# Kernel optimization log

Measured on AMD Instinct MI355X. Metric: run time of the kernel, lower is better.

## Reference

```python
import jax, jax.numpy as jnp
import numpy as np

K_NEIGHBORS = 3


def setup_inputs() -> dict:
    key = jax.random.key(0)
    ks = jax.random.split(key, 16)
    B, N = 8, 2048
    s = 0.05
    p = {
        "x": jax.random.normal(ks[0], (B, N, 4), dtype=jnp.float32),
        "W1": jax.random.normal(ks[1], (4, 64), dtype=jnp.float32) * s,
        "b1": jnp.zeros((64,), jnp.float32),
        "W2": jax.random.normal(ks[2], (64, 64), dtype=jnp.float32) * s,
        "b2": jnp.zeros((64,), jnp.float32),
        "Wm": jax.random.normal(ks[3], (64, 64), dtype=jnp.float32) * s,
        "bm": jnp.zeros((64,), jnp.float32),
        "Wu1": jax.random.normal(ks[4], (128, 128), dtype=jnp.float32) * s,
        "bu1": jnp.zeros((128,), jnp.float32),
        "Wu2": jax.random.normal(ks[5], (128, 128), dtype=jnp.float32) * s,
        "bu2": jnp.zeros((128,), jnp.float32),
        "Wmean": jax.random.normal(ks[6], (128, 2), dtype=jnp.float32) * s,
        "bmean": jnp.zeros((2,), jnp.float32),
        "Wv": jax.random.normal(ks[7], (128, 1), dtype=jnp.float32) * s,
        "bv": jnp.zeros((1,), jnp.float32),
        "log_std": jnp.zeros((2,), jnp.float32),
    }
    return p


def reference(x, W1, b1, W2, b2, Wm, bm, Wu1, bu1, Wu2, bu2, Wmean, bmean, Wv, bv, log_std):
    # node MLP: [B,N,4] -> [B,N,64]
    h = jax.nn.relu(x @ W1 + b1)
    h = jax.nn.relu(h @ W2 + b2)
    # pairwise squared distances without materializing [B,N,N,64] diff:
    # ||a-b||^2 = ||a||^2 + ||b||^2 - 2 a.b  (same math as diff.pow(2).sum(-1))
    sq = jnp.sum(h * h, axis=-1)  # [B,N]
    gram = jnp.einsum("bnd,bmd->bnm", h, h)  # [B,N,N]
    dist = sq[:, :, None] + sq[:, None, :] - 2.0 * gram  # [B,N,N]
    # k smallest (ascending) = top_k of negated dist; drop self (index 0)
    _, idx = jax.lax.top_k(-dist, K_NEIGHBORS + 1)  # [B,N,K+1]
    knn_idx = idx[:, :, 1:]  # [B,N,K]
    # gather neighbor features: [B,N,K,64]
    neigh = jax.vmap(lambda hb, ib: hb[ib])(h, knn_idx)
    # msg MLP + mean over neighbors
    msgs = jax.nn.relu(neigh @ Wm + bm).mean(axis=2)  # [B,N,64]
    hc = jnp.concatenate([h, msgs], axis=-1)  # [B,N,128]
    u = jax.nn.relu(hc @ Wu1 + bu1)
    u = jax.nn.relu(u @ Wu2 + bu2)
    return (u @ Wmean + bmean, jnp.exp(log_std), u @ Wv + bv)
```

## Files before the change

### kernel.cpp

```cpp
#include <hip/hip_runtime.h>
#include <math.h>

#define NB 8
#define NN 2048

typedef short bf16x8 __attribute__((ext_vector_type(8)));
typedef float f32x4  __attribute__((ext_vector_type(4)));

__device__ __forceinline__ f32x4 mfma16(uint4 a, uint4 b, f32x4 c) {
    return __builtin_amdgcn_mfma_f32_16x16x32_bf16(
        __builtin_bit_cast(bf16x8, a), __builtin_bit_cast(bf16x8, b), c, 0, 0, 0);
}

__device__ __forceinline__ float bf2f(unsigned short u) {
    unsigned int t = ((unsigned int)u) << 16;
    return __builtin_bit_cast(float, t);
}

__device__ __forceinline__ unsigned short f2bf_rne(float f) {
    unsigned int u = __builtin_bit_cast(unsigned int, f);
    return (unsigned short)((u + 0x7FFFu + ((u >> 16) & 1u)) >> 16);
}

__device__ __forceinline__ unsigned int rne_pair(unsigned int a, unsigned int b, unsigned int c) {
    float lo = bf2f((unsigned short)(a & 0xFFFF)) + bf2f((unsigned short)(b & 0xFFFF)) + bf2f((unsigned short)(c & 0xFFFF));
    float hi = bf2f((unsigned short)(a >> 16)) + bf2f((unsigned short)(b >> 16)) + bf2f((unsigned short)(c >> 16));
    return (unsigned int)f2bf_rne(lo) | ((unsigned int)f2bf_rne(hi) << 16);
}
__device__ __forceinline__ uint4 rne_merge(uint4 a, uint4 b, uint4 c) {
    return make_uint4(rne_pair(a.x, b.x, c.x), rne_pair(a.y, b.y, c.y),
                      rne_pair(a.z, b.z, c.z), rne_pair(a.w, b.w, c.w));
}

#define INS4(vv, ii, d, j) {                                      \
    bool c0 = (d < vv.x) || (d == vv.x && j < ii.x);              \
    bool c1 = (d < vv.y) || (d == vv.y && j < ii.y);              \
    bool c2 = (d < vv.z) || (d == vv.z && j < ii.z);              \
    bool c3 = (d < vv.w) || (d == vv.w && j < ii.w);              \
    vv.w = c3 ? (c2 ? vv.z : d) : vv.w; ii.w = c3 ? (c2 ? ii.z : j) : ii.w; \
    vv.z = c2 ? (c1 ? vv.y : d) : vv.z; ii.z = c2 ? (c1 ? ii.y : j) : ii.z; \
    vv.y = c1 ? (c0 ? vv.x : d) : vv.y; ii.y = c1 ? (c0 ? ii.x : j) : ii.y; \
    vv.x = c0 ? d : vv.x;               ii.x = c0 ? j : ii.x; }

#define INS4S(vv, ii, d, j) {                                     \
    bool c0 = (d < vv.x); bool c1 = (d < vv.y);                   \
    bool c2 = (d < vv.z); bool c3 = (d < vv.w);                   \
    vv.w = c3 ? (c2 ? vv.z : d) : vv.w; ii.w = c3 ? (c2 ? ii.z : j) : ii.w; \
    vv.z = c2 ? (c1 ? vv.y : d) : vv.z; ii.z = c2 ? (c1 ? ii.y : j) : ii.z; \
    vv.y = c1 ? (c0 ? vv.x : d) : vv.y; ii.y = c1 ? (c0 ? ii.x : j) : ii.y; \
    vv.x = c0 ? d : vv.x;               ii.x = c0 ? j : ii.x; }

__global__ __launch_bounds__(256) void k_embed(
    const float* __restrict__ x, const float* __restrict__ W1, const float* __restrict__ b1,
    const float* __restrict__ W2, const float* __restrict__ b2,
    uint4* __restrict__ HsF, float* __restrict__ sqv)
{
    __shared__ float w2s[4096];
    __shared__ float h1s[4][4][64];
    __shared__ unsigned short sh[3 * 16 * 72];
    int tid = threadIdx.x;
    for (int q = tid; q < 4096; q += 256) w2s[q] = W2[q];
    int wave = tid >> 6, lane = tid & 63;
    int nbase = blockIdx.x * 16 + wave * 4;
    float w10 = W1[lane], w11 = W1[64 + lane], w12 = W1[128 + lane], w13 = W1[192 + lane];
    float b1l = b1[lane];
    #pragma unroll
    for (int v = 0; v < 4; v++) {
        float4 xv = reinterpret_cast<const float4*>(x)[nbase + v];
        h1s[wave][v][lane] = fmaxf(b1l + xv.x * w10 + xv.y * w11 + xv.z * w12 + xv.w * w13, 0.f);
    }
    __syncthreads();
    float b2l = b2[lane];
    float a0 = b2l, a1 = b2l, a2 = b2l, a3 = b2l;
    for (int k = 0; k < 64; k++) {
        float w = w2s[k * 64 + lane];
        a0 += h1s[wave][0][k] * w; a1 += h1s[wave][1][k] * w;
        a2 += h1s[wave][2][k] * w; a3 += h1s[wave][3][k] * w;
    }
    float hvs[4] = {fmaxf(a0, 0.f), fmaxf(a1, 0.f), fmaxf(a2, 0.f), fmaxf(a3, 0.f)};
    #pragma unroll
    for (int v = 0; v < 4; v++) {
        float hval = hvs[v];
        long node = nbase + v;
        int row = wave * 4 + v;
        unsigned int u0 = __builtin_bit_cast(unsigned int, hval);
        unsigned short s0 = (unsigned short)(u0 >> 16);
        float f0 = __builtin_bit_cast(float, u0 & 0xFFFF0000u);
        float r1 = hval - f0;
        unsigned int u1 = __builtin_bit_cast(unsigned int, r1);
        unsigned short s1 = (unsigned short)(u1 >> 16);
        float f1 = __builtin_bit_cast(float, u1 & 0xFFFF0000u);
        float r2 = r1 - f1;
        unsigned short s2 = (unsigned short)(__builtin_bit_cast(unsigned int, r2) >> 16);
        sh[(0 * 16 + row) * 72 + lane] = s0;
        sh[(1 * 16 + row) * 72 + lane] = s1;
        sh[(2 * 16 + row) * 72 + lane] = s2;
        float s = hval * hval;
        #pragma unroll
        for (int m = 1; m < 64; m <<= 1) s += __shfl_xor(s, m, 64);
        if (lane == 0) sqv[node] = s;
    }
    __syncthreads();
    for (int q = tid; q < 384; q += 256) {
        int f = q >> 6, ln = q & 63;
        int s = f >> 1, hf = f & 1;
        int row = ln & 15, eb = hf * 32 + (ln >> 4) * 8;
        const unsigned short* sp = &sh[(s * 16 + row) * 72 + eb];
        unsigned int p0 = (unsigned int)sp[0] | ((unsigned int)sp[1] << 16);
        unsigned int p1 = (unsigned int)sp[2] | ((unsigned int)sp[3] << 16);
        unsigned int p2 = (unsigned int)sp[4] | ((unsigned int)sp[5] << 16);
        unsigned int p3 = (unsigned int)sp[6] | ((unsigned int)sp[7] << 16);
        HsF[((long)blockIdx.x * 6 + f) * 64 + ln] = make_uint4(p0, p1, p2, p3);
    }
}

__global__ __launch_bounds__(256, 3) void k_knn(
    const uint4* __restrict__ HsF, const float* __restrict__ sqv,
    float* __restrict__ pval, int* __restrict__ pidx)
{
    __shared__ float smv[4][1056];
    __shared__ int   smi[4][1056];

    int tid = threadIdx.x;
    int wave = tid >> 6, lane = tid & 63;
    int l15 = lane & 15, quad = lane >> 4;

    int bx = blockIdx.x;
    int js = bx & 3;
    int gquad = (bx >> 2) & 31;
    int b = bx >> 7;
    int gwb = gquad * 4 + wave;
    long g = (long)b * 128 + gwb;
    const float* sqb = sqv + ((long)b << 11);

    uint4 A[6];
    #pragma unroll
    for (int f = 0; f < 6; f++)
        A[f] = HsF[(g * 6 + f) * 64 + lane];

    float4 val[4]; int4 idx[4];
    #pragma unroll
    for (int r = 0; r < 4; r++) {
        val[r] = make_float4(3.4e38f, 3.4e38f, 3.4e38f, 3.4e38f);
        idx[r] = make_int4(0x7fffffff, 0x7fffffff, 0x7fffffff, 0x7fffffff);
    }

#define LOADB(B, SJ, G) {                                                     \
    long fb = ((long)b * 128 + (G)) * 6;                                      \
    _Pragma("unroll")                                                         \
    for (int f = 0; f < 6; f++)                                               \
        B[f] = HsF[(fb + f) * 64 + lane];                                     \
    SJ = sqb[(G) * 16 + l15]; }

#define COMPUTE(B, SJ, G) {                                                   \
    int j = (G) * 16 + l15;                                                   \
    f32x4 acc = {0.f, 0.f, 0.f, 0.f};                                         \
    _Pragma("unroll")                                                         \
    for (int hf = 0; hf < 2; hf++) {                                          \
        acc = mfma16(A[hf],     B[hf],     acc);                              \
        acc = mfma16(A[hf],     B[2 + hf], acc);                              \
        acc = mfma16(A[2 + hf], B[hf],     acc);                              \
        acc = mfma16(A[2 + hf], B[2 + hf], acc);                              \
        acc = mfma16(A[hf],     B[4 + hf], acc);                              \
        acc = mfma16(A[4 + hf], B[hf],     acc);                              \
    }                                                                         \
    _Pragma("unroll")                                                         \
    for (int r = 0; r < 4; r++) {                                             \
        float d = fmaf(-2.f, acc[r], SJ);                                     \
        INS4S(val[r], idx[r], d, j);                                          \
    } }

    int jg0 = js * 32;
    uint4 B0[6], B1[6];
    float sj0, sj1;
    LOADB(B0, sj0, jg0);
    #pragma unroll 1
    for (int t = 0; t < 16; t++) {
        int ga = jg0 + t * 2;
        int gbn = ga + 1;
        int gc = jg0 + ((t * 2 + 2) & 31);
        LOADB(B1, sj1, gbn);
        COMPUTE(B0, sj0, ga);
        LOADB(B0, sj0, gc);
        COMPUTE(B1, sj1, gbn);
    }

    float* mv = smv[wave]; int* mi = smi[wave];
    #pragma unroll
    for (int r = 0; r < 4; r++) {
        int base = (quad * 4 + r) * 65 + l15 * 4;
        mv[base + 0] = val[r].x; mv[base + 1] = val[r].y;
        mv[base + 2] = val[r].z; mv[base + 3] = val[r].w;
        mi[base + 0] = idx[r].x; mi[base + 1] = idx[r].y;
        mi[base + 2] = idx[r].z; mi[base + 3] = idx[r].w;
    }
    __syncthreads();
    float4 fv = make_float4(3.4e38f, 3.4e38f, 3.4e38f, 3.4e38f);
    int4   fi = make_int4(0x7fffffff, 0x7fffffff, 0x7fffffff, 0x7fffffff);
    #pragma unroll
    for (int tt = 0; tt < 4; tt++) {
        int base = l15 * 65 + (quad * 4 + tt) * 4;
        #pragma unroll
        for (int k = 0; k < 4; k++) {
            float d = mv[base + k];
            int j = mi[base + k];
            INS4(fv, fi, d, j);
        }
    }
    #pragma unroll
    for (int m = 16; m <= 32; m <<= 1) {
        float ov0 = __shfl_xor(fv.x, m, 64), ov1 = __shfl_xor(fv.y, m, 64);
        float ov2 = __shfl_xor(fv.z, m, 64), ov3 = __shfl_xor(fv.w, m, 64);
        int   oi0 = __shfl_xor(fi.x, m, 64), oi1 = __shfl_xor(fi.y, m, 64);
        int   oi2 = __shfl_xor(fi.z, m, 64), oi3 = __shfl_xor(fi.w, m, 64);
        INS4(fv, fi, ov0, oi0); INS4(fv, fi, ov1, oi1);
        INS4(fv, fi, ov2, oi2); INS4(fv, fi, ov3, oi3);
    }
    if (quad == 0) {
        long gi = ((long)b << 11) + gwb * 16 + l15;
        pval[gi * 16 + js * 4 + 0] = fv.x; pidx[gi * 16 + js * 4 + 0] = fi.x;
        pval[gi * 16 + js * 4 + 1] = fv.y; pidx[gi * 16 + js * 4 + 1] = fi.y;
        pval[gi * 16 + js * 4 + 2] = fv.z; pidx[gi * 16 + js * 4 + 2] = fi.z;
        pval[gi * 16 + js * 4 + 3] = fv.w; pidx[gi * 16 + js * 4 + 3] = fi.w;
    }
}

__global__ __launch_bounds__(256) void k_knn_merge(
    const float* __restrict__ pval, const int* __restrict__ pidx, int* __restrict__ knn)
{
    int gi = blockIdx.x * 256 + threadIdx.x;
    float4 fv = make_float4(3.4e38f, 3.4e38f, 3.4e38f, 3.4e38f);
    int4   fi = make_int4(0x7fffffff, 0x7fffffff, 0x7fffffff, 0x7fffffff);
    #pragma unroll
    for (int t = 0; t < 16; t++) {
        float d = pval[(long)gi * 16 + t];
        int j = pidx[(long)gi * 16 + t];
        INS4(fv, fi, d, j);
    }
    int* o = knn + (long)gi * 3;
    o[0] = fi.y; o[1] = fi.z; o[2] = fi.w;
}

__global__ __launch_bounds__(256) void k_head(
    const uint4* __restrict__ HsF, const int* __restrict__ knn,
    const float* __restrict__ Wm, const float* __restrict__ bm,
    const float* __restrict__ Wu1, const float* __restrict__ bu1,
    const float* __restrict__ Wu2, const float* __restrict__ bu2,
    const float* __restrict__ Wmean, const float* __restrict__ bmean,
    const float* __restrict__ Wv, const float* __restrict__ bv,
    const float* __restrict__ log_std,
    float* __restrict__ out_mean, float* __restrict__ out_std, float* __restrict__ out_val)
{
    __shared__ __align__(16) uint4 wmf[8 * 64];
    __shared__ __align__(16) uint4 wuf[32 * 64];
    __shared__ __align__(16) unsigned short hcT[4][16 * 136];

    int tid = threadIdx.x;
    int wave = tid >> 6, lane = tid & 63;
    int l15 = lane & 15, quad = lane >> 4;
    long g = blockIdx.x * 4 + wave;
    int b = (int)(g >> 7);

    for (int q = tid; q < 512; q += 256) {
        int fi2 = q >> 6, ln = q & 63;
        int fg = fi2 >> 1, hf = fi2 & 1;
        int fr = ln & 15, qd = ln >> 4;
        unsigned int p[4];
        #pragma unroll
        for (int e2 = 0; e2 < 4; e2++) {
            unsigned int lo = f2bf_rne(Wm[(hf * 32 + qd * 8 + e2 * 2 + 0) * 64 + fg * 16 + fr]);
            unsigned int hi = f2bf_rne(Wm[(hf * 32 + qd * 8 + e2 * 2 + 1) * 64 + fg * 16 + fr]);
            p[e2] = lo | (hi << 16);
        }
        wmf[q] = make_uint4(p[0], p[1], p[2], p[3]);
    }
#define STAGE_WU(W) {                                                         \
    for (int q = tid; q < 2048; q += 256) {                                   \
        int fi2 = q >> 6, ln = q & 63;                                        \
        int fg = fi2 >> 2, kq = fi2 & 3;                                      \
        int fr = ln & 15, qd = ln >> 4;                                       \
        unsigned int p[4];                                                    \
        _Pragma("unroll")                                                     \
        for (int e2 = 0; e2 < 4; e2++) {                                      \
            unsigned int lo = f2bf_rne(W[(kq * 32 + qd * 8 + e2 * 2 + 0) * 128 + fg * 16 + fr]); \
            unsigned int hi = f2bf_rne(W[(kq * 32 + qd * 8 + e2 * 2 + 1) * 128 + fg * 16 + fr]); \
            p[e2] = lo | (hi << 16);                                          \
        }                                                                     \
        wuf[q] = make_uint4(p[0], p[1], p[2], p[3]);                          \
    } }
    STAGE_WU(Wu1)

    uint4 hA[2];
    #pragma unroll
    for (int hf = 0; hf < 2; hf++)
        hA[hf] = rne_merge(HsF[(g * 6 + hf) * 64 + lane],
                           HsF[(g * 6 + 2 + hf) * 64 + lane],
                           HsF[(g * 6 + 4 + hf) * 64 + lane]);
    uint4 nA[3][2];
    {
        int node0 = (int)g * 16 + l15;
        #pragma unroll
        for (int e = 0; e < 3; e++) {
            int jn = knn[node0 * 3 + e];
            long gj = (long)b * 128 + (jn >> 4);
            int ln2 = quad * 16 + (jn & 15);
            #pragma unroll
            for (int hf = 0; hf < 2; hf++)
                nA[e][hf] = rne_merge(HsF[(gj * 6 + hf) * 64 + ln2],
                                      HsF[(gj * 6 + 2 + hf) * 64 + ln2],
                                      HsF[(gj * 6 + 4 + hf) * 64 + ln2]);
        }
    }
    #pragma unroll
    for (int hf = 0; hf < 2; hf++)
        *reinterpret_cast<uint4*>(&hcT[wave][l15 * 136 + hf * 32 + quad * 8]) = hA[hf];
    __syncthreads();

    {
        uint4 wm_r[4][2];
        #pragma unroll
        for (int fg = 0; fg < 4; fg++)
            #pragma unroll
            for (int hf = 0; hf < 2; hf++)
                wm_r[fg][hf] = wmf[(fg * 2 + hf) * 64 + lane];
        float bmv[4];
        #pragma unroll
        for (int fg = 0; fg < 4; fg++) bmv[fg] = bm[fg * 16 + l15];
        f32x4 msum[4];
        #pragma unroll
        for (int fg = 0; fg < 4; fg++) msum[fg] = (f32x4){0.f, 0.f, 0.f, 0.f};
        #pragma unroll
        for (int e = 0; e < 3; e++)
            #pragma unroll
            for (int fg = 0; fg < 4; fg++) {
                f32x4 c = {0.f, 0.f, 0.f, 0.f};
                c = mfma16(nA[e][0], wm_r[fg][0], c);
                c = mfma16(nA[e][1], wm_r[fg][1], c);
                #pragma unroll
                for (int r = 0; r < 4; r++) msum[fg][r] += fmaxf(c[r] + bmv[fg], 0.f);
            }
        #pragma unroll
        for (int fg = 0; fg < 4; fg++)
            #pragma unroll
            for (int r = 0; r < 4; r++)
                hcT[wave][(quad * 4 + r) * 136 + 64 + fg * 16 + l15] = f2bf_rne(msum[fg][r] * (1.f / 3.f));
    }
    __syncthreads();

    unsigned short u1s[8][4];
    {
        uint4 a1[4];
        #pragma unroll
        for (int kq = 0; kq < 4; kq++)
            a1[kq] = *reinterpret_cast<const uint4*>(&hcT[wave][l15 * 136 + kq * 32 + quad * 8]);
        #pragma unroll
        for (int fg = 0; fg < 8; fg++) {
            float bv1 = bu1[fg * 16 + l15];
            f32x4 c = {0.f, 0.f, 0.f, 0.f};
            #pragma unroll
            for (int kq = 0; kq < 4; kq++)
                c = mfma16(a1[kq], wuf[(fg * 4 + kq) * 64 + lane], c);
            #pragma unroll
            for (int r = 0; r < 4; r++) u1s[fg][r] = f2bf_rne(fmaxf(c[r] + bv1, 0.f));
        }
        #pragma unroll
        for (int fg = 0; fg < 8; fg++)
            #pragma unroll
            for (int r = 0; r < 4; r++)
                hcT[wave][(quad * 4 + r) * 136 + fg * 16 + l15] = u1s[fg][r];
    }
    __syncthreads();
    STAGE_WU(Wu2)
    __syncthreads();

    float u2v[8][4];
    {
        uint4 a2[4];
        #pragma unroll
        for (int kq = 0; kq < 4; kq++)
            a2[kq] = *reinterpret_cast<const uint4*>(&hcT[wave][l15 * 136 + kq * 32 + quad * 8]);
        #pragma unroll
        for (int fg = 0; fg < 8; fg++) {
            float bv2 = bu2[fg * 16 + l15];
            f32x4 c = {0.f, 0.f, 0.f, 0.f};
            #pragma unroll
            for (int kq = 0; kq < 4; kq++)
                c = mfma16(a2[kq], wuf[(fg * 4 + kq) * 64 + lane], c);
            #pragma unroll
            for (int r = 0; r < 4; r++) u2v[fg][r] = fmaxf(c[r] + bv2, 0.f);
        }
    }

    {
        float wm0[8], wm1[8], wvv[8];
        #pragma unroll
        for (int fg = 0; fg < 8; fg++) {
            int f = fg * 16 + l15;
            wm0[fg] = Wmean[f * 2 + 0];
            wm1[fg] = Wmean[f * 2 + 1];
            wvv[fg] = Wv[f];
        }
        float bm0 = bmean[0], bm1 = bmean[1], bv0 = bv[0];
        #pragma unroll
        for (int r = 0; r < 4; r++) {
            float p0 = 0.f, p1 = 0.f, p2 = 0.f;
            #pragma unroll
            for (int fg = 0; fg < 8; fg++) {
                p0 = fmaf(u2v[fg][r], wm0[fg], p0);
                p1 = fmaf(u2v[fg][r], wm1[fg], p1);
                p2 = fmaf(u2v[fg][r], wvv[fg], p2);
            }
            #pragma unroll
            for (int m = 1; m < 16; m <<= 1) {
                p0 += __shfl_xor(p0, m, 64);
                p1 += __shfl_xor(p1, m, 64);
                p2 += __shfl_xor(p2, m, 64);
            }
            if (l15 == 0) {
                int node = (int)g * 16 + quad * 4 + r;
                out_mean[node * 2 + 0] = p0 + bm0;
                out_mean[node * 2 + 1] = p1 + bm1;
                out_val[node] = p2 + bv0;
            }
        }
    }
    if (blockIdx.x == 0 && tid < 2) out_std[tid] = expf(log_std[tid]);
}

extern "C" void kernel_launch(void* const* d_in, const int* in_sizes, int n_in,
                              void* d_out, int out_size, void* d_ws, size_t ws_size,
                              hipStream_t stream) {
    const float* x     = (const float*)d_in[0];
    const float* W1    = (const float*)d_in[1];
    const float* b1    = (const float*)d_in[2];
    const float* W2    = (const float*)d_in[3];
    const float* b2    = (const float*)d_in[4];
    const float* Wm    = (const float*)d_in[5];
    const float* bm    = (const float*)d_in[6];
    const float* Wu1   = (const float*)d_in[7];
    const float* bu1   = (const float*)d_in[8];
    const float* Wu2   = (const float*)d_in[9];
    const float* bu2   = (const float*)d_in[10];
    const float* Wmean = (const float*)d_in[11];
    const float* bmean = (const float*)d_in[12];
    const float* Wv    = (const float*)d_in[13];
    const float* bv    = (const float*)d_in[14];
    const float* lstd  = (const float*)d_in[15];

    float* out = (float*)d_out;
    float* out_mean = out;
    float* out_std  = out + 32768;
    float* out_val  = out + 32770;

    uint4* HsF  = (uint4*)d_ws;
    float* sqv  = (float*)(HsF + (long)1024 * 6 * 64);
    int*   knn  = (int*)(sqv + 16384);
    float* pval = (float*)(knn + 16384 * 3);
    int*   pidx = (int*)(pval + (long)16384 * 16);

    k_embed<<<1024, 256, 0, stream>>>(x, W1, b1, W2, b2, HsF, sqv);
    k_knn<<<1024, 256, 0, stream>>>(HsF, sqv, pval, pidx);
    k_knn_merge<<<64, 256, 0, stream>>>(pval, pidx, knn);
    k_head<<<256, 256, 0, stream>>>(HsF, knn, Wm, bm, Wu1, bu1, Wu2, bu2,
                                    Wmean, bmean, Wv, bv, lstd,
                                    out_mean, out_std, out_val);
}
```

Baseline: 203.5 us.

## Fold kNN merge into head, pre-convert weights once, use shuffle-based top-4 reduction

Removes the separate k_knn_merge kernel. The kNN kernel now reduces its per-lane top-4 lists with xor shuffles instead of a shared-memory transpose and writes packed 64-bit (distance key, index) pairs. k_head merges the four partial lists with u64 comparisons and shuffles. Weight bf16 fragment conversion moves from every head block into a small prep kernel, and k_head reads the fragments from global memory instead of LDS. The kNN inner loop is now fully unrolled with no explicit double-buffering, which raises register pressure. The packed sort key keeps the tie-break by index.

```diff
diff --git a/kernel.cpp b/kernel.cpp
--- a/kernel.cpp
+++ b/kernel.cpp
@@ -6,6 +6,7 @@
 
 typedef short bf16x8 __attribute__((ext_vector_type(8)));
 typedef float f32x4  __attribute__((ext_vector_type(4)));
+typedef unsigned long long u64;
 
 __device__ __forceinline__ f32x4 mfma16(uint4 a, uint4 b, f32x4 c) {
     return __builtin_amdgcn_mfma_f32_16x16x32_bf16(
@@ -30,6 +31,12 @@
 __device__ __forceinline__ uint4 rne_merge(uint4 a, uint4 b, uint4 c) {
     return make_uint4(rne_pair(a.x, b.x, c.x), rne_pair(a.y, b.y, c.y),
                       rne_pair(a.z, b.z, c.z), rne_pair(a.w, b.w, c.w));
+}
+
+__device__ __forceinline__ u64 packdj(float d, int j) {
+    unsigned int u = __builtin_bit_cast(unsigned int, d);
+    unsigned int key = u ^ ((unsigned int)(((int)u) >> 31) | 0x80000000u);
+    return ((u64)key << 32) | (unsigned int)j;
 }
 
 #define INS4(vv, ii, d, j) {                                      \
@@ -49,6 +56,47 @@
     vv.z = c2 ? (c1 ? vv.y : d) : vv.z; ii.z = c2 ? (c1 ? ii.y : j) : ii.z; \
     vv.y = c1 ? (c0 ? vv.x : d) : vv.y; ii.y = c1 ? (c0 ? ii.x : j) : ii.y; \
     vv.x = c0 ? d : vv.x;               ii.x = c0 ? j : ii.x; }
+
+#define INSQ(a0, a1, a2, a3, p) {                                 \
+    bool c0 = (p) < a0; bool c1 = (p) < a1;                       \
+    bool c2 = (p) < a2; bool c3 = (p) < a3;                       \
+    a3 = c3 ? (c2 ? a2 : (p)) : a3;                               \
+    a2 = c2 ? (c1 ? a1 : (p)) : a2;                               \
+    a1 = c1 ? (c0 ? a0 : (p)) : a1;                               \
+    a0 = c0 ? (p) : a0; }
+
+__global__ __launch_bounds__(256) void k_wprep(
+    const float* __restrict__ Wm, const float* __restrict__ Wu1, const float* __restrict__ Wu2,
+    uint4* __restrict__ wfrag)
+{
+    int q = blockIdx.x * 256 + threadIdx.x;
+    int ln = q & 63;
+    int fr = ln & 15, qd = ln >> 4;
+    unsigned int p[4];
+    if (q < 512) {
+        int fi2 = q >> 6;
+        int fg = fi2 >> 1, hf = fi2 & 1;
+        #pragma unroll
+        for (int e2 = 0; e2 < 4; e2++) {
+            unsigned int lo = f2bf_rne(Wm[(hf * 32 + qd * 8 + e2 * 2 + 0) * 64 + fg * 16 + fr]);
+            unsigned int hi = f2bf_rne(Wm[(hf * 32 + qd * 8 + e2 * 2 + 1) * 64 + fg * 16 + fr]);
+            p[e2] = lo | (hi << 16);
+        }
+    } else {
+        int qq = q - 512;
+        const float* W = (qq < 2048) ? Wu1 : Wu2;
+        int q2 = qq & 2047;
+        int fi2 = q2 >> 6;
+        int fg = fi2 >> 2, kq = fi2 & 3;
+        #pragma unroll
+        for (int e2 = 0; e2 < 4; e2++) {
+            unsigned int lo = f2bf_rne(W[(kq * 32 + qd * 8 + e2 * 2 + 0) * 128 + fg * 16 + fr]);
+            unsigned int hi = f2bf_rne(W[(kq * 32 + qd * 8 + e2 * 2 + 1) * 128 + fg * 16 + fr]);
+            p[e2] = lo | (hi << 16);
+        }
+    }
+    wfrag[q] = make_uint4(p[0], p[1], p[2], p[3]);
+}
 
 __global__ __launch_bounds__(256) void k_embed(
     const float* __restrict__ x, const float* __restrict__ W1, const float* __restrict__ b1,
@@ -116,11 +164,8 @@
 
 __global__ __launch_bounds__(256, 3) void k_knn(
     const uint4* __restrict__ HsF, const float* __restrict__ sqv,
-    float* __restrict__ pval, int* __restrict__ pidx)
+    u64* __restrict__ pk)
 {
-    __shared__ float smv[4][1056];
-    __shared__ int   smi[4][1056];
-
     int tid = threadIdx.x;
     int wave = tid >> 6, lane = tid & 63;
     int l15 = lane & 15, quad = lane >> 4;
@@ -145,114 +190,68 @@
         idx[r] = make_int4(0x7fffffff, 0x7fffffff, 0x7fffffff, 0x7fffffff);
     }
 
-#define LOADB(B, SJ, G) {                                                     \
-    long fb = ((long)b * 128 + (G)) * 6;                                      \
-    _Pragma("unroll")                                                         \
-    for (int f = 0; f < 6; f++)                                               \
-        B[f] = HsF[(fb + f) * 64 + lane];                                     \
-    SJ = sqb[(G) * 16 + l15]; }
-
-#define COMPUTE(B, SJ, G) {                                                   \
-    int j = (G) * 16 + l15;                                                   \
-    f32x4 acc = {0.f, 0.f, 0.f, 0.f};                                         \
-    _Pragma("unroll")                                                         \
-    for (int hf = 0; hf < 2; hf++) {                                          \
-        acc = mfma16(A[hf],     B[hf],     acc);                              \
-        acc = mfma16(A[hf],     B[2 + hf], acc);                              \
-        acc = mfma16(A[2 + hf], B[hf],     acc);                              \
-        acc = mfma16(A[2 + hf], B[2 + hf], acc);                              \
-        acc = mfma16(A[hf],     B[4 + hf], acc);                              \
-        acc = mfma16(A[4 + hf], B[hf],     acc);                              \
-    }                                                                         \
-    _Pragma("unroll")                                                         \
-    for (int r = 0; r < 4; r++) {                                             \
-        float d = fmaf(-2.f, acc[r], SJ);                                     \
-        INS4S(val[r], idx[r], d, j);                                          \
-    } }
-
     int jg0 = js * 32;
-    uint4 B0[6], B1[6];
-    float sj0, sj1;
-    LOADB(B0, sj0, jg0);
-    #pragma unroll 1
-    for (int t = 0; t < 16; t++) {
-        int ga = jg0 + t * 2;
-        int gbn = ga + 1;
-        int gc = jg0 + ((t * 2 + 2) & 31);
-        LOADB(B1, sj1, gbn);
-        COMPUTE(B0, sj0, ga);
-        LOADB(B0, sj0, gc);
-        COMPUTE(B1, sj1, gbn);
-    }
-
-    float* mv = smv[wave]; int* mi = smi[wave];
-    #pragma unroll
-    for (int r = 0; r < 4; r++) {
-        int base = (quad * 4 + r) * 65 + l15 * 4;
-        mv[base + 0] = val[r].x; mv[base + 1] = val[r].y;
-        mv[base + 2] = val[r].z; mv[base + 3] = val[r].w;
-        mi[base + 0] = idx[r].x; mi[base + 1] = idx[r].y;
-        mi[base + 2] = idx[r].z; mi[base + 3] = idx[r].w;
-    }
-    __syncthreads();
-    float4 fv = make_float4(3.4e38f, 3.4e38f, 3.4e38f, 3.4e38f);
-    int4   fi = make_int4(0x7fffffff, 0x7fffffff, 0x7fffffff, 0x7fffffff);
-    #pragma unroll
-    for (int tt = 0; tt < 4; tt++) {
-        int base = l15 * 65 + (quad * 4 + tt) * 4;
-        #pragma unroll
-        for (int k = 0; k < 4; k++) {
-            float d = mv[base + k];
-            int j = mi[base + k];
-            INS4(fv, fi, d, j);
-        }
-    }
-    #pragma unroll
-    for (int m = 16; m <= 32; m <<= 1) {
-        float ov0 = __shfl_xor(fv.x, m, 64), ov1 = __shfl_xor(fv.y, m, 64);
-        float ov2 = __shfl_xor(fv.z, m, 64), ov3 = __shfl_xor(fv.w, m, 64);
-        int   oi0 = __shfl_xor(fi.x, m, 64), oi1 = __shfl_xor(fi.y, m, 64);
-        int   oi2 = __shfl_xor(fi.z, m, 64), oi3 = __shfl_xor(fi.w, m, 64);
-        INS4(fv, fi, ov0, oi0); INS4(fv, fi, ov1, oi1);
-        INS4(fv, fi, ov2, oi2); INS4(fv, fi, ov3, oi3);
-    }
-    if (quad == 0) {
-        long gi = ((long)b << 11) + gwb * 16 + l15;
-        pval[gi * 16 + js * 4 + 0] = fv.x; pidx[gi * 16 + js * 4 + 0] = fi.x;
-        pval[gi * 16 + js * 4 + 1] = fv.y; pidx[gi * 16 + js * 4 + 1] = fi.y;
-        pval[gi * 16 + js * 4 + 2] = fv.z; pidx[gi * 16 + js * 4 + 2] = fi.z;
-        pval[gi * 16 + js * 4 + 3] = fv.w; pidx[gi * 16 + js * 4 + 3] = fi.w;
-    }
-}
-
-__global__ __launch_bounds__(256) void k_knn_merge(
-    const float* __restrict__ pval, const int* __restrict__ pidx, int* __restrict__ knn)
-{
-    int gi = blockIdx.x * 256 + threadIdx.x;
-    float4 fv = make_float4(3.4e38f, 3.4e38f, 3.4e38f, 3.4e38f);
-    int4   fi = make_int4(0x7fffffff, 0x7fffffff, 0x7fffffff, 0x7fffffff);
-    #pragma unroll
-    for (int t = 0; t < 16; t++) {
-        float d = pval[(long)gi * 16 + t];
-        int j = pidx[(long)gi * 16 + t];
-        INS4(fv, fi, d, j);
-    }
-    int* o = knn + (long)gi * 3;
-    o[0] = fi.y; o[1] = fi.z; o[2] = fi.w;
+    #pragma unroll
+    for (int t = 0; t < 32; t++) {
+        int G = jg0 + t;
+        long fb = ((long)b * 128 + G) * 6;
+        uint4 B[6];
+        #pragma unroll
+        for (int f = 0; f < 6; f++)
+            B[f] = HsF[(fb + f) * 64 + lane];
+        float sj = sqb[G * 16 + l15];
+
+        f32x4 acc = {0.f, 0.f, 0.f, 0.f};
+        #pragma unroll
+        for (int hf = 0; hf < 2; hf++) {
+            acc = mfma16(A[hf],     B[hf],     acc);
+            acc = mfma16(A[hf],     B[2 + hf], acc);
+            acc = mfma16(A[2 + hf], B[hf],     acc);
+            acc = mfma16(A[2 + hf], B[2 + hf], acc);
+            acc = mfma16(A[hf],     B[4 + hf], acc);
+            acc = mfma16(A[4 + hf], B[hf],     acc);
+        }
+        int j = G * 16 + l15;
+        #pragma unroll
+        for (int r = 0; r < 4; r++) {
+            float d = fmaf(-2.f, acc[r], sj);
+            INS4S(val[r], idx[r], d, j);
+        }
+    }
+
+    #pragma unroll
+    for (int m = 1; m <= 8; m <<= 1) {
+        #pragma unroll
+        for (int r = 0; r < 4; r++) {
+            float ov0 = __shfl_xor(val[r].x, m, 64), ov1 = __shfl_xor(val[r].y, m, 64);
+            float ov2 = __shfl_xor(val[r].z, m, 64), ov3 = __shfl_xor(val[r].w, m, 64);
+            int   oi0 = __shfl_xor(idx[r].x, m, 64), oi1 = __shfl_xor(idx[r].y, m, 64);
+            int   oi2 = __shfl_xor(idx[r].z, m, 64), oi3 = __shfl_xor(idx[r].w, m, 64);
+            INS4(val[r], idx[r], ov0, oi0); INS4(val[r], idx[r], ov1, oi1);
+            INS4(val[r], idx[r], ov2, oi2); INS4(val[r], idx[r], ov3, oi3);
+        }
+    }
+    if (l15 == 0) {
+        #pragma unroll
+        for (int r = 0; r < 4; r++) {
+            long node = ((long)b << 11) + gwb * 16 + quad * 4 + r;
+            u64* dst = pk + node * 16 + js * 4;
+            reinterpret_cast<ulonglong2*>(dst)[0] =
+                make_ulonglong2(packdj(val[r].x, idx[r].x), packdj(val[r].y, idx[r].y));
+            reinterpret_cast<ulonglong2*>(dst)[1] =
+                make_ulonglong2(packdj(val[r].z, idx[r].z), packdj(val[r].w, idx[r].w));
+        }
+    }
 }
 
 __global__ __launch_bounds__(256) void k_head(
-    const uint4* __restrict__ HsF, const int* __restrict__ knn,
-    const float* __restrict__ Wm, const float* __restrict__ bm,
-    const float* __restrict__ Wu1, const float* __restrict__ bu1,
-    const float* __restrict__ Wu2, const float* __restrict__ bu2,
+    const uint4* __restrict__ HsF, const u64* __restrict__ pk, const uint4* __restrict__ wfrag,
+    const float* __restrict__ bm, const float* __restrict__ bu1, const float* __restrict__ bu2,
     const float* __restrict__ Wmean, const float* __restrict__ bmean,
     const float* __restrict__ Wv, const float* __restrict__ bv,
     const float* __restrict__ log_std,
     float* __restrict__ out_mean, float* __restrict__ out_std, float* __restrict__ out_val)
 {
-    __shared__ __align__(16) uint4 wmf[8 * 64];
-    __shared__ __align__(16) uint4 wuf[32 * 64];
     __shared__ __align__(16) unsigned short hcT[4][16 * 136];
 
     int tid = threadIdx.x;
@@ -261,34 +260,23 @@
     long g = blockIdx.x * 4 + wave;
     int b = (int)(g >> 7);
 
-    for (int q = tid; q < 512; q += 256) {
-        int fi2 = q >> 6, ln = q & 63;
-        int fg = fi2 >> 1, hf = fi2 & 1;
-        int fr = ln & 15, qd = ln >> 4;
-        unsigned int p[4];
-        #pragma unroll
-        for (int e2 = 0; e2 < 4; e2++) {
-            unsigned int lo = f2bf_rne(Wm[(hf * 32 + qd * 8 + e2 * 2 + 0) * 64 + fg * 16 + fr]);
-            unsigned int hi = f2bf_rne(Wm[(hf * 32 + qd * 8 + e2 * 2 + 1) * 64 + fg * 16 + fr]);
-            p[e2] = lo | (hi << 16);
-        }
-        wmf[q] = make_uint4(p[0], p[1], p[2], p[3]);
-    }
-#define STAGE_WU(W) {                                                         \
-    for (int q = tid; q < 2048; q += 256) {                                   \
-        int fi2 = q >> 6, ln = q & 63;                                        \
-        int fg = fi2 >> 2, kq = fi2 & 3;                                      \
-        int fr = ln & 15, qd = ln >> 4;                                       \
-        unsigned int p[4];                                                    \
-        _Pragma("unroll")                                                     \
-        for (int e2 = 0; e2 < 4; e2++) {                                      \
-            unsigned int lo = f2bf_rne(W[(kq * 32 + qd * 8 + e2 * 2 + 0) * 128 + fg * 16 + fr]); \
-            unsigned int hi = f2bf_rne(W[(kq * 32 + qd * 8 + e2 * 2 + 1) * 128 + fg * 16 + fr]); \
-            p[e2] = lo | (hi << 16);                                          \
-        }                                                                     \
-        wuf[q] = make_uint4(p[0], p[1], p[2], p[3]);                          \
-    } }
-    STAGE_WU(Wu1)
+    int nb[3];
+    {
+        const u64* src = pk + ((long)g * 16 + l15) * 16 + quad * 4;
+        ulonglong2 a01 = reinterpret_cast<const ulonglong2*>(src)[0];
+        ulonglong2 a23 = reinterpret_cast<const ulonglong2*>(src)[1];
+        u64 m0 = a01.x, m1 = a01.y, m2 = a23.x, m3 = a23.y;
+        #pragma unroll
+        for (int m = 16; m <= 32; m <<= 1) {
+            u64 p0 = __shfl_xor(m0, m, 64), p1 = __shfl_xor(m1, m, 64);
+            u64 p2 = __shfl_xor(m2, m, 64), p3 = __shfl_xor(m3, m, 64);
+            INSQ(m0, m1, m2, m3, p0); INSQ(m0, m1, m2, m3, p1);
+            INSQ(m0, m1, m2, m3, p2); INSQ(m0, m1, m2, m3, p3);
+        }
+        nb[0] = (int)(unsigned int)m1;
+        nb[1] = (int)(unsigned int)m2;
+        nb[2] = (int)(unsigned int)m3;
+    }
 
     uint4 hA[2];
     #pragma unroll
@@ -297,19 +285,16 @@
                            HsF[(g * 6 + 2 + hf) * 64 + lane],
                            HsF[(g * 6 + 4 + hf) * 64 + lane]);
     uint4 nA[3][2];
-    {
-        int node0 = (int)g * 16 + l15;
-        #pragma unroll
-        for (int e = 0; e < 3; e++) {
-            int jn = knn[node0 * 3 + e];
-            long gj = (long)b * 128 + (jn >> 4);
-            int ln2 = quad * 16 + (jn & 15);
-            #pragma unroll
-            for (int hf = 0; hf < 2; hf++)
-                nA[e][hf] = rne_merge(HsF[(gj * 6 + hf) * 64 + ln2],
-                                      HsF[(gj * 6 + 2 + hf) * 64 + ln2],
-                                      HsF[(gj * 6 + 4 + hf) * 64 + ln2]);
-        }
+    #pragma unroll
+    for (int e = 0; e < 3; e++) {
+        int jn = nb[e];
+        long gj = (long)b * 128 + (jn >> 4);
+        int ln2 = quad * 16 + (jn & 15);
+        #pragma unroll
+        for (int hf = 0; hf < 2; hf++)
+            nA[e][hf] = rne_merge(HsF[(gj * 6 + hf) * 64 + ln2],
+                                  HsF[(gj * 6 + 2 + hf) * 64 + ln2],
+                                  HsF[(gj * 6 + 4 + hf) * 64 + ln2]);
     }
     #pragma unroll
     for (int hf = 0; hf < 2; hf++)
@@ -322,7 +307,7 @@
         for (int fg = 0; fg < 4; fg++)
             #pragma unroll
             for (int hf = 0; hf < 2; hf++)
-                wm_r[fg][hf] = wmf[(fg * 2 + hf) * 64 + lane];
+                wm_r[fg][hf] = wfrag[(fg * 2 + hf) * 64 + lane];
         float bmv[4];
         #pragma unroll
         for (int fg = 0; fg < 4; fg++) bmv[fg] = bm[fg * 16 + l15];
@@ -347,30 +332,29 @@
     }
     __syncthreads();
 
-    unsigned short u1s[8][4];
     {
         uint4 a1[4];
         #pragma unroll
         for (int kq = 0; kq < 4; kq++)
             a1[kq] = *reinterpret_cast<const uint4*>(&hcT[wave][l15 * 136 + kq * 32 + quad * 8]);
+        unsigned short u1s[8][4];
         #pragma unroll
         for (int fg = 0; fg < 8; fg++) {
             float bv1 = bu1[fg * 16 + l15];
             f32x4 c = {0.f, 0.f, 0.f, 0.f};
             #pragma unroll
             for (int kq = 0; kq < 4; kq++)
-                c = mfma16(a1[kq], wuf[(fg * 4 + kq) * 64 + lane], c);
+                c = mfma16(a1[kq], wfrag[512 + (fg * 4 + kq) * 64 + lane], c);
             #pragma unroll
             for (int r = 0; r < 4; r++) u1s[fg][r] = f2bf_rne(fmaxf(c[r] + bv1, 0.f));
         }
+        __syncthreads();
         #pragma unroll
         for (int fg = 0; fg < 8; fg++)
             #pragma unroll
             for (int r = 0; r < 4; r++)
                 hcT[wave][(quad * 4 + r) * 136 + fg * 16 + l15] = u1s[fg][r];
     }
-    __syncthreads();
-    STAGE_WU(Wu2)
     __syncthreads();
 
     float u2v[8][4];
@@ -385,7 +369,7 @@
             f32x4 c = {0.f, 0.f, 0.f, 0.f};
             #pragma unroll
             for (int kq = 0; kq < 4; kq++)
-                c = mfma16(a2[kq], wuf[(fg * 4 + kq) * 64 + lane], c);
+                c = mfma16(a2[kq], wfrag[2560 + (fg * 4 + kq) * 64 + lane], c);
             #pragma unroll
             for (int r = 0; r < 4; r++) u2v[fg][r] = fmaxf(c[r] + bv2, 0.f);
         }
@@ -452,16 +436,15 @@
     float* out_std  = out + 32768;
     float* out_val  = out + 32770;
 
-    uint4* HsF  = (uint4*)d_ws;
-    float* sqv  = (float*)(HsF + (long)1024 * 6 * 64);
-    int*   knn  = (int*)(sqv + 16384);
-    float* pval = (float*)(knn + 16384 * 3);
-    int*   pidx = (int*)(pval + (long)16384 * 16);
-
+    uint4* HsF   = (uint4*)d_ws;
+    float* sqv   = (float*)(HsF + (long)1024 * 6 * 64);
+    uint4* wfrag = (uint4*)(sqv + 16384);
+    u64*   pk    = (u64*)(wfrag + 4608);
+
+    k_wprep<<<18, 256, 0, stream>>>(Wm, Wu1, Wu2, wfrag);
     k_embed<<<1024, 256, 0, stream>>>(x, W1, b1, W2, b2, HsF, sqv);
-    k_knn<<<1024, 256, 0, stream>>>(HsF, sqv, pval, pidx);
-    k_knn_merge<<<64, 256, 0, stream>>>(pval, pidx, knn);
-    k_head<<<256, 256, 0, stream>>>(HsF, knn, Wm, bm, Wu1, bu1, Wu2, bu2,
+    k_knn<<<1024, 256, 0, stream>>>(HsF, sqv, pk);
+    k_head<<<256, 256, 0, stream>>>(HsF, pk, wfrag, bm, bu1, bu2,
                                     Wmean, bmean, Wv, bv, lstd,
                                     out_mean, out_std, out_val);
 }
```

Measured after the change: 665.8 us. 227% more time.
